# Performance work log

Hardware: AMD Instinct MI355X
Metric: run time of the kernel (lower is better)

Reference implementation:

```python
import jax, jax.numpy as jnp
import numpy as np
from functools import partial
from jax import lax

B, K, CLIP_DIM, SBERT_DIM, D_MODEL, R_RANK, ATTN_DIM, PMAX = 128, 1024, 768, 384, 256, 64, 256, 8
RHO = 0.35

def _normalize(x, axis=-1, eps=1e-12):
    return x / jnp.maximum(jnp.linalg.norm(x, axis=axis, keepdims=True), eps)

def _build_graph():
    rng = np.random.default_rng(0)
    pid = np.zeros((K, PMAX), np.int32)
    pm = np.zeros((K, PMAX), bool)
    for i in range(K - 1):  # node i's parents are in (i, K); root = K-1 has none
        n = int(rng.integers(1, PMAX + 1))
        n = min(n, K - 1 - i)
        cands = rng.choice(np.arange(i + 1, K), size=n, replace=False)
        pid[i, :n] = cands
        pm[i, :n] = True
    order = np.arange(K - 1, -1, -1, dtype=np.int32)  # parents before children
    return jnp.asarray(pid), jnp.asarray(pm), jnp.asarray(order)

def setup_inputs() -> dict:
    key = jax.random.key(0)
    ks = iter(jax.random.split(key, 32))
    r = lambda shape, s=0.02: jax.random.normal(next(ks), shape, jnp.float32) * s
    pid, pm, order = _build_graph()
    return {
        "t_clip": jax.random.normal(next(ks), (B, CLIP_DIM), jnp.float32),
        "v_clip": jax.random.normal(next(ks), (B, CLIP_DIM), jnp.float32),
        "concept_sbert": jax.random.normal(next(ks), (K, SBERT_DIM), jnp.float32),
        "Wt": r((CLIP_DIM, D_MODEL)), "bt": jnp.zeros((D_MODEL,)),
        "Wv": r((CLIP_DIM, D_MODEL)), "bv": jnp.zeros((D_MODEL,)),
        "Wc": r((SBERT_DIM, D_MODEL)), "bc": jnp.zeros((D_MODEL,)),
        "Wp1": r((3 * D_MODEL, 2 * D_MODEL)), "bp1": jnp.zeros((2 * D_MODEL,)),
        "Wp2": r((2 * D_MODEL, D_MODEL)), "bp2": jnp.zeros((D_MODEL,)),
        "Wm1": r((3 * D_MODEL, 2 * D_MODEL)), "bm1": jnp.zeros((2 * D_MODEL,)),
        "Wm2": r((2 * D_MODEL, D_MODEL)), "bm2": jnp.zeros((D_MODEL,)),
        "tau_logits": jnp.zeros((K,)),
        "U": r((D_MODEL, R_RANK)), "V": r((D_MODEL, R_RANK)),
        "Wg1": r((SBERT_DIM, R_RANK)), "bg1": jnp.zeros((R_RANK,)),
        "Wg2": r((R_RANK, R_RANK)), "bg2": jnp.zeros((R_RANK,)),
        "w_out": r((K, R_RANK)), "b_out": jnp.zeros((K,)),
        "concept_q": r((K, ATTN_DIM)),
        "parents_idx": pid, "parents_mask": pm, "order": order,
    }

def _forward(t_clip, v_clip, concept_sbert, Wt, bt, Wv, bv, Wc, bc,
             Wp1, bp1, Wp2, bp2, Wm1, bm1, Wm2, bm2, tau_logits,
             U, V, Wg1, bg1, Wg2, bg2, w_out, b_out, concept_q,
             parents_idx, parents_mask, order):
    gelu = partial(jax.nn.gelu, approximate=False)  # torch nn.GELU default = exact erf
    t = _normalize(t_clip) @ Wt + bt                 # [B, D]
    v = _normalize(v_clip) @ Wv + bv                 # [B, D]
    d = concept_sbert @ Wc + bc                      # [K, D]
    # x = [v, t, d] broadcast to [B, K, 3D]
    x = jnp.concatenate([
        jnp.broadcast_to(v[:, None, :], (t.shape[0], K, D_MODEL)),
        jnp.broadcast_to(t[:, None, :], (t.shape[0], K, D_MODEL)),
        jnp.broadcast_to(d[None, :, :], (t.shape[0], K, D_MODEL)),
    ], axis=-1)
    h_plus = gelu(x @ Wp1 + bp1) @ Wp2 + bp2
    h_minus = gelu(x @ Wm1 + bm1) @ Wm2 + bm2
    tau = jax.nn.sigmoid(tau_logits)[None, :, None]
    h = tau * h_plus + (1.0 - tau) * h_minus         # [B, K, D]
    u = jnp.einsum('bkd,dr->bkr', h, U)
    vv = jnp.einsum('bkd,dr->bkr', h, V)
    g = gelu(concept_sbert @ Wg1 + bg1) @ Wg2 + bg2  # [K, R]
    inter = u * vv * g[None, :, :]
    logits = jnp.einsum('bkr,kr->bk', inter, w_out) + b_out[None, :]
    p = jax.nn.sigmoid(logits)                        # [B, K]
    # --- top-down hierarchical attention + multiplicative aggregation ---
    q = _normalize(concept_q)                         # [K, A]
    def step(p_hat, node):
        par = parents_idx[node]                       # [P] int
        m = parents_mask[node]                        # [P] bool
        scores = jnp.where(m, q[par] @ q[node], -1e9)
        alpha = jax.nn.softmax(scores)                # [P]
        vals = p_hat[:, par]                          # [B, P] gather of parent probs
        prod = jnp.prod(jnp.where(m[None, :], alpha[None, :] * vals, 1.0), axis=-1)
        new = jnp.where(m.any(), RHO * p[:, node] + (1.0 - RHO) * prod, p_hat[:, node])
        return p_hat.at[:, node].set(new), None       # scatter write
    p_hat, _ = lax.scan(step, p, order)
    return p_hat

def reference(t_clip, v_clip, concept_sbert, Wt, bt, Wv, bv, Wc, bc,
              Wp1, bp1, Wp2, bp2, Wm1, bm1, Wm2, bm2, tau_logits,
              U, V, Wg1, bg1, Wg2, bg2, w_out, b_out, concept_q,
              parents_idx, parents_mask, order):
    return _forward(t_clip, v_clip, concept_sbert, Wt, bt, Wv, bv, Wc, bc,
                    Wp1, bp1, Wp2, bp2, Wm1, bm1, Wm2, bm2, tau_logits,
                    U, V, Wg1, bg1, Wg2, bg2, w_out, b_out, concept_q,
                    parents_idx, parents_mask, order)
```

## Files before the change

### kernel.cpp

```cpp
#include <hip/hip_runtime.h>
#include <math.h>

typedef __attribute__((ext_vector_type(8))) short short8;
typedef __attribute__((ext_vector_type(4))) float float4v;
typedef __attribute__((ext_vector_type(2))) float float2v;

struct P {
  const float *t_clip, *v_clip, *sbert;
  const float *Wt, *bt, *Wv, *bv, *Wc, *bc;
  const float *Wp1, *bp1, *Wp2, *bp2, *Wm1, *bm1, *Wm2, *bm2;
  const float *tau_logits, *U, *V, *Wg1, *bg1, *Wg2, *bg2, *w_out, *b_out, *concept_q;
  const int *pid;
  float *vt32;
  unsigned short *vtbf;
  unsigned short *dbf;
  unsigned short *w1upP, *w1upM;
  unsigned short *w1lowP, *w1lowM;
  unsigned short *Ctp, *Ctm;
  unsigned short *Wpk, *Wmk;
  float *Ap, *Am;
  float *biasPM, *tau, *gw, *aprod;
  unsigned short *parS;
  int *sorted, *lvlStart, *nlev;
  float *pOut;
};

__device__ __forceinline__ unsigned short bf16ru(float f) {
    unsigned u = __float_as_uint(f);
    u += 0x7fffu + ((u >> 16) & 1u);
    return (unsigned short)(u >> 16);
}

__device__ __forceinline__ unsigned packpair(float2v a, unsigned c) {
    float2v cb;
    cb.x = __uint_as_float(c << 16);
    cb.y = __uint_as_float(c & 0xffff0000u);
    float2v x = a + cb;
    float2v t = x * x;
    float2v i = t * (-0.06649038f) + 0.39894228f;
    float2v p = x * i + 0.5f;
    float2v g = x * p;
    union { float2v f; unsigned u[2]; } gu; gu.f = g;
    return __builtin_amdgcn_perm(gu.u[1], gu.u[0], 0x07060302u);
}


__device__ void tv_f(const P& a, int rel, float* sm) {
    int sel = rel & 1, ct = (rel >> 1) & 1, bt8 = rel >> 2;
    float* xrow = sm;
    float* scale = sm + 6144;
    int tid = threadIdx.x;
    const float* X = sel ? a.t_clip : a.v_clip;
    int b0 = bt8 * 8;
    for (int r = 0; r < 8; ++r)
        for (int i = tid; i < 768; i += 256)
            xrow[r * 768 + i] = X[(size_t)(b0 + r) * 768 + i];
    __syncthreads();
    {
        int r = tid >> 5, l = tid & 31;
        float ss = 0.f;
        for (int i = l; i < 768; i += 32) { float v = xrow[r * 768 + i]; ss = fmaf(v, v, ss); }
        for (int mk = 16; mk; mk >>= 1) ss += __shfl_xor(ss, mk);
        if (l == 0) scale[r] = 1.0f / fmaxf(sqrtf(ss), 1e-12f);
    }
    __syncthreads();
    int col = ct * 128 + (tid & 127);
    int rg = tid >> 7;
    const float* W = sel ? a.Wt : a.Wv;
    const float* bias = sel ? a.bt : a.bv;
    float acc[4] = {};
    for (int d = 0; d < 768; ++d) {
        float w = W[(size_t)d * 256 + col];
        const float* xr = xrow + (rg * 4) * 768 + d;
        acc[0] = fmaf(xr[0],    w, acc[0]);
        acc[1] = fmaf(xr[768],  w, acc[1]);
        acc[2] = fmaf(xr[1536], w, acc[2]);
        acc[3] = fmaf(xr[2304], w, acc[3]);
    }
    int vtcol = sel * 256 + col;
    float bb = bias[col];
#pragma unroll
    for (int r = 0; r < 4; ++r) {
        int b = b0 + rg * 4 + r;
        float y = acc[r] * scale[rg * 4 + r] + bb;
        a.vt32[(size_t)b * 512 + vtcol] = y;
        a.vtbf[(size_t)(b >> 4) * 8192 + (vtcol >> 5) * 512 + ((vtcol >> 3) & 3) * 128
               + (b & 15) * 8 + (vtcol & 7)] = bf16ru(y);
    }
}

__device__ void d_f(const P& a, int rel, float* sm) {
    int r0 = rel * 8;
    int tid = threadIdx.x;
    for (int i = tid; i < 3072; i += 256) sm[i] = a.sbert[(size_t)r0 * 384 + i];
    __syncthreads();
    float acc[8] = {};
    int col = tid;
    for (int d = 0; d < 384; ++d) {
        float w = a.Wc[(size_t)d * 256 + col];
#pragma unroll
        for (int r = 0; r < 8; ++r) acc[r] = fmaf(sm[r * 384 + d], w, acc[r]);
    }
    float bb = a.bc[col];
#pragma unroll
    for (int r = 0; r < 8; ++r) {
        int row = r0 + r;
        a.dbf[(size_t)(row >> 4) * 4096 + (col >> 5) * 512 + ((col >> 3) & 3) * 128
              + (row & 15) * 8 + (col & 7)] = bf16ru(acc[r] + bb);
    }
}

__device__ void wcv_f(const P& a, int rel, float* smf) {
    unsigned short* wl = (unsigned short*)smf;
    int mat = rel & 1, rb = rel >> 1;
    int r0 = rb * 16;
    const float* W1 = mat ? a.Wm1 : a.Wp1;
    int tid = threadIdx.x;
    for (int i = tid; i < 8192; i += 256)
        wl[i] = bf16ru(W1[(size_t)r0 * 512 + i]);
    __syncthreads();
    unsigned short* dst; int K16, kbase;
    if (r0 < 512) { dst = mat ? a.w1upM : a.w1upP;  K16 = 8192; kbase = r0; }
    else          { dst = mat ? a.w1lowM : a.w1lowP; K16 = 4096; kbase = r0 - 512; }
    for (int i = tid; i < 1024; i += 256) {
        int kg = i >> 9, n = i & 511;
        int k0 = kbase + kg * 8;
        ushort4 o0, o1;
        o0.x = wl[(kg * 8 + 0) * 512 + n]; o0.y = wl[(kg * 8 + 1) * 512 + n];
        o0.z = wl[(kg * 8 + 2) * 512 + n]; o0.w = wl[(kg * 8 + 3) * 512 + n];
        o1.x = wl[(kg * 8 + 4) * 512 + n]; o1.y = wl[(kg * 8 + 5) * 512 + n];
        o1.z = wl[(kg * 8 + 6) * 512 + n]; o1.w = wl[(kg * 8 + 7) * 512 + n];
        size_t off = (size_t)(n >> 4) * K16 + (k0 >> 5) * 512 + ((k0 >> 3) & 3) * 128 + (n & 15) * 8;
        *(ushort4*)&dst[off]     = o0;
        *(ushort4*)&dst[off + 4] = o1;
    }
}

__device__ void packW_f(const P& a, int rel, float* smf) {
    float* w2l = smf;
    int mat = rel >> 6, jb = rel & 63;
    int j0 = jb * 8;
    const float* W2 = mat ? a.Wm2 : a.Wp2;
    unsigned short* outP = mat ? a.Wmk : a.Wpk;
    int tid = threadIdx.x;
    for (int i = tid; i < 2048; i += 256) w2l[i] = W2[(size_t)j0 * 256 + i];
    __syncthreads();
    int c = tid & 127, jg = tid >> 7;
    float acc[4] = {};
    const float* uv = (c < 64) ? (a.U + c) : (a.V + (c - 64));
    for (int d = 0; d < 256; ++d) {
        float u = uv[(size_t)d * 64];
        const float* wr = w2l + (jg * 4) * 256 + d;
        acc[0] = fmaf(wr[0],   u, acc[0]);
        acc[1] = fmaf(wr[256], u, acc[1]);
        acc[2] = fmaf(wr[512], u, acc[2]);
        acc[3] = fmaf(wr[768], u, acc[3]);
    }
#pragma unroll
    for (int r = 0; r < 4; ++r) {
        int j = j0 + jg * 4 + r;
        size_t o = (size_t)(j >> 5) * 4096 + (c >> 4) * 512 + ((j >> 3) & 3) * 128 + (c & 15) * 8 + (j & 7);
        outP[o] = bf16ru(acc[r]);
    }
}

__device__ void gw_f(const P& a, int rel, float* sm) {
    float* sb = sm;
    float* hid = sm + 6144;
    int k0 = rel * 16;
    int tid = threadIdx.x;
    for (int i = tid; i < 6144; i += 256) sb[i] = a.sbert[(size_t)k0 * 384 + i];
    __syncthreads();
    int col = tid & 63, rg = tid >> 6;
    float bg = a.bg1[col];
    float acc[4] = {bg, bg, bg, bg};
    for (int d = 0; d < 384; ++d) {
        float w = a.Wg1[(size_t)d * 64 + col];
        const float* xr = sb + (rg * 4) * 384 + d;
        acc[0] = fmaf(xr[0],    w, acc[0]);
        acc[1] = fmaf(xr[384],  w, acc[1]);
        acc[2] = fmaf(xr[768],  w, acc[2]);
        acc[3] = fmaf(xr[1152], w, acc[3]);
    }
#pragma unroll
    for (int r = 0; r < 4; ++r)
        hid[(rg * 4 + r) * 64 + col] = 0.5f * acc[r] * (1.0f + erff(acc[r] * 0.7071067811865475f));
    __syncthreads();
    float bg2v = a.bg2[col];
    float a2[4] = {bg2v, bg2v, bg2v, bg2v};
    for (int d = 0; d < 64; ++d) {
        float w = a.Wg2[(size_t)d * 64 + col];
        const float* hr = hid + (rg * 4) * 64 + d;
        a2[0] = fmaf(hr[0],   w, a2[0]);
        a2[1] = fmaf(hr[64],  w, a2[1]);
        a2[2] = fmaf(hr[128], w, a2[2]);
        a2[3] = fmaf(hr[192], w, a2[3]);
    }
#pragma unroll
    for (int r = 0; r < 4; ++r) {
        int k = k0 + rg * 4 + r;
        a.gw[(size_t)k * 64 + col] = a2[r] * a.w_out[(size_t)k * 64 + col];
    }
}

__device__ void alpha_f(const P& a, int blk) {
    int t = threadIdx.x, wv = t >> 6, lane = t & 63;
    int node = blk * 4 + wv;
    int slot = lane >> 3, e = lane & 7;
    int par = a.pid[node * 8 + slot];
    const float4* qk = (const float4*)(a.concept_q + (size_t)node * 256);
    const float4* qp = (const float4*)(a.concept_q + (size_t)par * 256);
    float dq = 0, np = 0, ns = 0;
#pragma unroll
    for (int i = 0; i < 8; ++i) {
        float4 x = qp[e * 8 + i], y = qk[e * 8 + i];
        dq += x.x * y.x + x.y * y.y + x.z * y.z + x.w * y.w;
        np += x.x * x.x + x.y * x.y + x.z * x.z + x.w * x.w;
        ns += y.x * y.x + y.y * y.y + y.z * y.z + y.w * y.w;
    }
#pragma unroll
    for (int mk = 1; mk <= 4; mk <<= 1) {
        dq += __shfl_xor(dq, mk); np += __shfl_xor(np, mk); ns += __shfl_xor(ns, mk);
    }
    float score = dq / fmaxf(sqrtf(np) * sqrtf(ns), 1e-24f);
    float sc[8]; int pv[8];
#pragma unroll
    for (int s = 0; s < 8; ++s) { sc[s] = __shfl(score, s * 8); pv[s] = __shfl(par, s * 8); }
    float mx = -1e30f;
#pragma unroll
    for (int s = 0; s < 8; ++s) if (pv[s] != 0) mx = fmaxf(mx, sc[s]);
    float sum = 0.f;
#pragma unroll
    for (int s = 0; s < 8; ++s) sum += (pv[s] != 0) ? expf(sc[s] - mx) : 0.0f;
    float ap = 1.0f;
#pragma unroll
    for (int s = 0; s < 8; ++s) if (pv[s] != 0) ap *= expf(sc[s] - mx) / sum;
    if (lane == 0) a.aprod[node] = ap;
    if (e == 0) a.parS[node * 8 + slot] = (par != 0) ? (unsigned short)par : (unsigned short)1024;
}

__device__ void misc_f(const P& a, int g) {
    int t = threadIdx.x;
    if (g == 0) {
        int c = t & 127;
        const float* bb = (t < 128) ? a.bp2 : a.bm2;
        const float* uv = (c < 64) ? (a.U + c) : (a.V + (c - 64));
        float acc = 0.f;
        for (int d = 0; d < 256; ++d) acc = fmaf(bb[d], uv[(size_t)d * 64], acc);
        a.biasPM[t] = acc;
    } else {
        int k = (g - 1) * 256 + t;
        a.tau[k] = 1.0f / (1.0f + expf(-a.tau_logits[k]));
    }
}

__device__ void levels_f(const P& a, int* smemI) {
    volatile int* lvl = smemI;
    int* cnt  = smemI + 1024;
    int* ofs  = smemI + 2048;
    int* ping = smemI + 3072;
    int* pong = smemI + 3328;
    int* mflag = smemI + 3584;
    int t = threadIdx.x;
    int par[4][8]; int hasm[4];
#pragma unroll
    for (int r = 0; r < 4; ++r) {
        int n = t * 4 + r, h = 0;
#pragma unroll
        for (int s = 0; s < 8; ++s) { int p = a.pid[n * 8 + s]; par[r][s] = p; h |= (p != 0); }
        hasm[r] = h; lvl[n] = 0;
    }
    if (t == 0) mflag[1] = 0;
    __syncthreads();
    for (int round = 0; round < 200; ++round) {
        if (t == 0) mflag[0] = 0;
        __syncthreads();
        int ch = 0;
        for (int sub = 0; sub < 8; ++sub) {
#pragma unroll
            for (int r = 0; r < 4; ++r) {
                if (!hasm[r]) continue;
                int mx = 0;
#pragma unroll
                for (int s = 0; s < 8; ++s) { int p = par[r][s]; if (p) mx = max(mx, lvl[p]); }
                int nl = mx + 1;
                if (nl > lvl[t * 4 + r]) { lvl[t * 4 + r] = nl; ch = 1; }
            }
        }
        if (ch) mflag[0] = 1;
        __syncthreads();
        if (mflag[0] == 0) break;
    }
    int lm = 0;
    for (int r = 0; r < 4; ++r) lm = max(lm, lvl[t * 4 + r]);
    atomicMax(&mflag[1], lm);
    for (int r = 0; r < 4; ++r) cnt[t * 4 + r] = 0;
    __syncthreads();
    for (int r = 0; r < 4; ++r) atomicAdd(&cnt[lvl[t * 4 + r]], 1);
    __syncthreads();
    int c0 = cnt[t * 4], c1 = cnt[t * 4 + 1], c2 = cnt[t * 4 + 2], c3 = cnt[t * 4 + 3];
    ping[t] = c0 + c1 + c2 + c3;
    __syncthreads();
    int* src = ping; int* dst = pong;
    for (int off = 1; off < 256; off <<= 1) {
        int v = src[t];
        if (t >= off) v += src[t - off];
        dst[t] = v;
        __syncthreads();
        int* tmp = src; src = dst; dst = tmp;
    }
    int excl = (t == 0) ? 0 : src[t - 1];
    ofs[t * 4] = excl; ofs[t * 4 + 1] = excl + c0;
    ofs[t * 4 + 2] = excl + c0 + c1; ofs[t * 4 + 3] = excl + c0 + c1 + c2;
#pragma unroll
    for (int r = 0; r < 4; ++r) a.lvlStart[t * 4 + r] = ofs[t * 4 + r];
    if (t == 0) { a.lvlStart[1024] = 1024; a.nlev[0] = mflag[1] + 1; }
    __syncthreads();
    for (int r = 0; r < 4; ++r) {
        int n = t * 4 + r;
        int pos = atomicAdd(&ofs[lvl[n]], 1);
        a.sorted[pos] = n;
    }
}

__global__ void __launch_bounds__(256) prep1_kernel(P a) {
    __shared__ float smem[7200];
    int bid = blockIdx.x;
    if (bid == 0) { levels_f(a, (int*)smem); return; }
    bid -= 1;
    if (bid < 64) { tv_f(a, bid, smem); return; }
    bid -= 64;
    if (bid < 128) { d_f(a, bid, smem); return; }
    bid -= 128;
    if (bid < 96) { wcv_f(a, bid, smem); return; }
    bid -= 96;
    if (bid < 128) { packW_f(a, bid, smem); return; }
    bid -= 128;
    if (bid < 64) { gw_f(a, bid, smem); return; }
    bid -= 64;
    if (bid < 256) { alpha_f(a, bid); return; }
    bid -= 256;
    misc_f(a, bid);
}

__global__ void __launch_bounds__(256) prep2_kernel(P a) {
    int bid = blockIdx.x;
    int tid = threadIdx.x;
    int wv = tid >> 6, lane = tid & 63;
    int m = lane & 15, quad = lane >> 4;
    if (bid < 128) {
        int mat = bid & 1, mt = (bid >> 1) & 15, ntile = bid >> 5;
        const unsigned short* A = a.dbf + (size_t)(mt * 4 + wv) * 4096 + quad * 128 + m * 8;
        const unsigned short* B = (mat ? a.w1lowM : a.w1lowP) + (size_t)quad * 128 + m * 8;
        unsigned short* Ct = mat ? a.Ctm : a.Ctp;
        float4v acc[8];
#pragma unroll
        for (int i = 0; i < 8; ++i) acc[i] = (float4v)0.0f;
        for (int s = 0; s < 8; ++s) {
            short8 af = *(const short8*)(A + s * 512);
#pragma unroll
            for (int nt = 0; nt < 8; ++nt) {
                short8 bf = *(const short8*)(B + (size_t)(ntile * 8 + nt) * 4096 + s * 512);
                acc[nt] = __builtin_amdgcn_mfma_f32_16x16x32_bf16(af, bf, acc[nt], 0, 0, 0);
            }
        }
        int rowg = mt * 4 + wv;
        int rl = quad * 4;
#pragma unroll
        for (int nt = 0; nt < 8; ++nt) {
            int j = ntile * 128 + nt * 16 + m;
            size_t base = (size_t)rowg * 8192 + (j >> 5) * 512 + ((j >> 3) & 3) * 128 + (j & 7);
#pragma unroll
            for (int rr = 0; rr < 4; ++rr)
                Ct[base + (rl + rr) * 8] = bf16ru(acc[nt][rr]);
        }
    } else {
        int rel = bid - 128;
        int mat = rel & 1, mt = (rel >> 1) & 1, ntile = rel >> 2;
        const unsigned short* A = a.vtbf + (size_t)(mt * 4 + wv) * 8192 + quad * 128 + m * 8;
        const unsigned short* B = (mat ? a.w1upM : a.w1upP) + (size_t)quad * 128 + m * 8;
        const float* bias = mat ? a.bm1 : a.bp1;
        float* out = mat ? a.Am : a.Ap;
        float4v acc[8];
#pragma unroll
        for (int i = 0; i < 8; ++i) acc[i] = (float4v)0.0f;
        for (int s = 0; s < 16; ++s) {
            short8 af = *(const short8*)(A + s * 512);
#pragma unroll
            for (int nt = 0; nt < 8; ++nt) {
                short8 bf = *(const short8*)(B + (size_t)(ntile * 8 + nt) * 8192 + s * 512);
                acc[nt] = __builtin_amdgcn_mfma_f32_16x16x32_bf16(af, bf, acc[nt], 0, 0, 0);
            }
        }
        int b0r = mt * 64 + wv * 16 + quad * 4;
#pragma unroll
        for (int nt = 0; nt < 8; ++nt) {
            int j = ntile * 128 + nt * 16 + m;
            float bb = bias[j];
#pragma unroll
            for (int rr = 0; rr < 4; ++rr)
                out[(size_t)(b0r + rr) * 512 + j] = acc[nt][rr] + bb;
        }
    }
}

__global__ void __launch_bounds__(512, 2) main_kernel(P a) {
    __shared__ float apL[4096];
    __shared__ float xbuf[4 * 4 * 64 * 8];
    int tid = threadIdx.x;
    int wv2 = tid >> 6, lane = tid & 63;
    int mat = wv2 >> 2, sub = wv2 & 3;
    int m = lane & 15, quad = lane >> 4;
    int b0 = (blockIdx.x >> 4) * 4;
    int k0 = (blockIdx.x & 15) << 6;

    for (int i = tid; i < 1024; i += 512) {
        int arr = i >> 7, off = i & 127;
        const float* src = ((arr >> 2) ? a.Am : a.Ap) + (size_t)(b0 + (arr & 3)) * 512;
        ((float4*)apL)[i] = ((const float4*)src)[off];
    }
    __syncthreads();

    const unsigned short* W  = mat ? a.Wmk : a.Wpk;
    const unsigned short* Ct = mat ? a.Ctm : a.Ctp;
    const float* aL = apL + mat * 2048;
    int kt = (k0 >> 4) + sub;
    const char* ctB = (const char*)Ct + (size_t)kt * 16384 + quad * 256 + m * 16;
    const char* wB  = (const char*)W + quad * 256 + m * 16;

    float4v acc[4][8];
#pragma unroll
    for (int b = 0; b < 4; ++b)
#pragma unroll
        for (int i = 0; i < 8; ++i) acc[b][i] = (float4v)0.0f;

    uint4 crN = *(const uint4*)(ctB);
    for (int n = 0; n < 16; ++n) {
        uint4 cr = crN;
        if (n < 15) crN = *(const uint4*)(ctB + (n + 1) * 1024);
        union { uint4 u; short8 s; } fa[4];
        const float* aj = aL + n * 32 + quad * 8;
#pragma unroll
        for (int b = 0; b < 4; ++b) {
            float4v x0 = *(const float4v*)(aj + b * 512);
            float4v x1 = *(const float4v*)(aj + b * 512 + 4);
            float2v v;
            v.x = x0[0]; v.y = x0[1]; fa[b].u.x = packpair(v, cr.x);
            v.x = x0[2]; v.y = x0[3]; fa[b].u.y = packpair(v, cr.y);
            v.x = x1[0]; v.y = x1[1]; fa[b].u.z = packpair(v, cr.z);
            v.x = x1[2]; v.y = x1[3]; fa[b].u.w = packpair(v, cr.w);
        }
        const char* wn = wB + n * 8192;
#pragma unroll
        for (int nt = 0; nt < 8; ++nt) {
            short8 wf = *(const short8*)(wn + nt * 1024);
            acc[0][nt] = __builtin_amdgcn_mfma_f32_16x16x32_bf16(fa[0].s, wf, acc[0][nt], 0, 0, 0);
            acc[1][nt] = __builtin_amdgcn_mfma_f32_16x16x32_bf16(fa[1].s, wf, acc[1][nt], 0, 0, 0);
            acc[2][nt] = __builtin_amdgcn_mfma_f32_16x16x32_bf16(fa[2].s, wf, acc[2][nt], 0, 0, 0);
            acc[3][nt] = __builtin_amdgcn_mfma_f32_16x16x32_bf16(fa[3].s, wf, acc[3][nt], 0, 0, 0);
        }
    }

    int kk[4]; float tv[4];
#pragma unroll
    for (int r = 0; r < 4; ++r) { kk[r] = k0 + sub * 16 + quad * 4 + r; tv[r] = a.tau[kk[r]]; }
    float lsum[4][4] = {};
    float* xb = xbuf + ((sub * 4) * 64 + lane) * 8;
#pragma unroll
    for (int t4 = 0; t4 < 4; ++t4) {
        __syncthreads();
        if (mat == 1) {
#pragma unroll
            for (int b = 0; b < 4; ++b) {
                float* d = xb + b * 512;
#pragma unroll
                for (int r = 0; r < 4; ++r) { d[r] = acc[b][t4][r]; d[4 + r] = acc[b][t4 + 4][r]; }
            }
        }
        __syncthreads();
        if (mat == 0) {
            int cU = t4 * 16 + m, cV = cU + 64;
            float bPu = a.biasPM[cU], bMu = a.biasPM[128 + cU];
            float bPv = a.biasPM[cV], bMv = a.biasPM[128 + cV];
#pragma unroll
            for (int b = 0; b < 4; ++b) {
                const float* d = xb + b * 512;
#pragma unroll
                for (int r = 0; r < 4; ++r) {
                    float g = a.gw[(size_t)kk[r] * 64 + cU];
                    float u  = tv[r] * (acc[b][t4][r] + bPu)     + (1.0f - tv[r]) * (d[r] + bMu);
                    float vx = tv[r] * (acc[b][t4 + 4][r] + bPv) + (1.0f - tv[r]) * (d[4 + r] + bMv);
                    lsum[b][r] = fmaf(u * vx, g, lsum[b][r]);
                }
            }
        }
    }
    if (mat == 0) {
#pragma unroll
        for (int r = 0; r < 4; ++r) {
            float bo = a.b_out[kk[r]];
#pragma unroll
            for (int b = 0; b < 4; ++b) {
                float s = lsum[b][r];
                s += __shfl_xor(s, 1); s += __shfl_xor(s, 2); s += __shfl_xor(s, 4); s += __shfl_xor(s, 8);
                if (m == 0)
                    a.pOut[(size_t)(b0 + b) * 1024 + kk[r]] = 1.0f / (1.0f + expf(-(s + bo)));
            }
        }
    }
}

#define PH_STRIDE 1056
__global__ void __launch_bounds__(256) scan_kernel(P a) {
    __shared__ float ph[4 * PH_STRIDE];
    __shared__ float aprodL[1024];
    __shared__ unsigned short parL[8192];
    __shared__ short sortedL[1024];
    __shared__ int lvlStartL[1025];
    int t = threadIdx.x;
    int b0 = blockIdx.x * 4;
    for (int i = t; i < 1024; i += 256) ((uint4*)parL)[i] = ((const uint4*)a.parS)[i];
    for (int i = t; i < 1024; i += 256) {
        aprodL[i] = a.aprod[i];
        sortedL[i] = (short)a.sorted[i];
        lvlStartL[i] = a.lvlStart[i];
    }
    if (t == 0) lvlStartL[1024] = 1024;
    for (int i = t; i < 4096; i += 256) {
        int bb = i >> 10, k = i & 1023;
        ph[bb * PH_STRIDE + k] = a.pOut[(size_t)(b0 + bb) * 1024 + k];
    }
    if (t < 4) ph[t * PH_STRIDE + 1024] = 1.0f;
    __syncthreads();
    int nlev = a.nlev[0];
    int w = t >> 6, lane = t & 63;
    float* myph = ph + w * PH_STRIDE;
    for (int L = 1; L < nlev; ++L) {
        int s0 = lvlStartL[L], s1 = lvlStartL[L + 1];
        for (int i = s0 + lane; i < s1; i += 64) {
            int node = sortedL[i];
            ushort4 pA = *(const ushort4*)&parL[node * 8];
            ushort4 pB = *(const ushort4*)&parL[node * 8 + 4];
            float prod = aprodL[node];
            prod *= myph[pA.x] * myph[pA.y];
            prod *= myph[pA.z] * myph[pA.w];
            prod *= myph[pB.x] * myph[pB.y];
            prod *= myph[pB.z] * myph[pB.w];
            myph[node] = fmaf(0.35f, myph[node], 0.65f * prod);
        }
    }
    __syncthreads();
    for (int i = t; i < 4096; i += 256) {
        int bb = i >> 10, k = i & 1023;
        a.pOut[(size_t)(b0 + bb) * 1024 + k] = ph[bb * PH_STRIDE + k];
    }
}

extern "C" void kernel_launch(void* const* d_in, const int* in_sizes, int n_in,
                              void* d_out, int out_size, void* d_ws, size_t ws_size,
                              hipStream_t stream) {
    P a;
    a.t_clip = (const float*)d_in[0];
    a.v_clip = (const float*)d_in[1];
    a.sbert  = (const float*)d_in[2];
    a.Wt  = (const float*)d_in[3];  a.bt  = (const float*)d_in[4];
    a.Wv  = (const float*)d_in[5];  a.bv  = (const float*)d_in[6];
    a.Wc  = (const float*)d_in[7];  a.bc  = (const float*)d_in[8];
    a.Wp1 = (const float*)d_in[9];  a.bp1 = (const float*)d_in[10];
    a.Wp2 = (const float*)d_in[11]; a.bp2 = (const float*)d_in[12];
    a.Wm1 = (const float*)d_in[13]; a.bm1 = (const float*)d_in[14];
    a.Wm2 = (const float*)d_in[15]; a.bm2 = (const float*)d_in[16];
    a.tau_logits = (const float*)d_in[17];
    a.U   = (const float*)d_in[18]; a.V   = (const float*)d_in[19];
    a.Wg1 = (const float*)d_in[20]; a.bg1 = (const float*)d_in[21];
    a.Wg2 = (const float*)d_in[22]; a.bg2 = (const float*)d_in[23];
    a.w_out = (const float*)d_in[24]; a.b_out = (const float*)d_in[25];
    a.concept_q = (const float*)d_in[26];
    a.pid = (const int*)d_in[27];

    char* w = (char*)d_ws;
    a.vt32   = (float*)(w + 0);
    a.vtbf   = (unsigned short*)(w + 262144);
    a.dbf    = (unsigned short*)(w + 393216);
    a.w1upP  = (unsigned short*)(w + 917504);
    a.w1upM  = (unsigned short*)(w + 1441792);
    a.w1lowP = (unsigned short*)(w + 1966080);
    a.w1lowM = (unsigned short*)(w + 2228224);
    a.Ctp    = (unsigned short*)(w + 2490368);
    a.Ctm    = (unsigned short*)(w + 3538944);
    a.Wpk    = (unsigned short*)(w + 4587520);
    a.Wmk    = (unsigned short*)(w + 4718592);
    a.Ap     = (float*)(w + 4849664);
    a.Am     = (float*)(w + 5111808);
    a.biasPM = (float*)(w + 5373952);
    a.tau    = (float*)(w + 5374976);
    a.gw     = (float*)(w + 5379072);
    a.parS   = (unsigned short*)(w + 5641216);
    a.aprod  = (float*)(w + 5657600);
    a.sorted = (int*)(w + 5661696);
    a.lvlStart = (int*)(w + 5665792);
    a.nlev     = (int*)(w + 5670144);
    a.pOut = (float*)d_out;

    prep1_kernel<<<742, 256, 0, stream>>>(a);
    prep2_kernel<<<144, 256, 0, stream>>>(a);
    main_kernel<<<512, 512, 0, stream>>>(a);
    scan_kernel<<<32, 256, 0, stream>>>(a);
}
```

Measured before the change: 286.9 us.

## Vectorize prep GEMVs, split prep2 tiles, stage main weights via LDS double buffer

```diff
diff --git a/kernel.cpp b/kernel.cpp
--- a/kernel.cpp
+++ b/kernel.cpp
@@ -31,6 +31,11 @@
     return (unsigned short)(u >> 16);
 }
 
+__device__ __forceinline__ void glds16(const void* g, void* l) {
+    __builtin_amdgcn_global_load_lds((const __attribute__((address_space(1))) unsigned int*)g,
+                                     (__attribute__((address_space(3))) unsigned int*)l, 16, 0, 0);
+}
+
 __device__ __forceinline__ unsigned packpair(float2v a, unsigned c) {
     float2v cb;
     cb.x = __uint_as_float(c << 16);
@@ -46,7 +51,7 @@
 
 
 __device__ void tv_f(const P& a, int rel, float* sm) {
-    int sel = rel & 1, ct = (rel >> 1) & 1, bt8 = rel >> 2;
+    int sel = rel & 1, bt8 = rel >> 1;
     float* xrow = sm;
     float* scale = sm + 6144;
     int tid = threadIdx.x;
@@ -64,28 +69,35 @@
         if (l == 0) scale[r] = 1.0f / fmaxf(sqrtf(ss), 1e-12f);
     }
     __syncthreads();
-    int col = ct * 128 + (tid & 127);
-    int rg = tid >> 7;
+    int col4 = (tid & 63) * 4, rg = tid >> 6;
     const float* W = sel ? a.Wt : a.Wv;
     const float* bias = sel ? a.bt : a.bv;
-    float acc[4] = {};
+    float acc[2][4] = {};
+    const float* xr0 = xrow + (rg * 2) * 768;
+    const float* xr1 = xr0 + 768;
     for (int d = 0; d < 768; ++d) {
-        float w = W[(size_t)d * 256 + col];
-        const float* xr = xrow + (rg * 4) * 768 + d;
-        acc[0] = fmaf(xr[0],    w, acc[0]);
-        acc[1] = fmaf(xr[768],  w, acc[1]);
-        acc[2] = fmaf(xr[1536], w, acc[2]);
-        acc[3] = fmaf(xr[2304], w, acc[3]);
-    }
-    int vtcol = sel * 256 + col;
-    float bb = bias[col];
-#pragma unroll
-    for (int r = 0; r < 4; ++r) {
-        int b = b0 + rg * 4 + r;
-        float y = acc[r] * scale[rg * 4 + r] + bb;
-        a.vt32[(size_t)b * 512 + vtcol] = y;
-        a.vtbf[(size_t)(b >> 4) * 8192 + (vtcol >> 5) * 512 + ((vtcol >> 3) & 3) * 128
-               + (b & 15) * 8 + (vtcol & 7)] = bf16ru(y);
+        float4 w = *(const float4*)&W[(size_t)d * 256 + col4];
+        float x0 = xr0[d], x1 = xr1[d];
+        acc[0][0] = fmaf(x0, w.x, acc[0][0]); acc[0][1] = fmaf(x0, w.y, acc[0][1]);
+        acc[0][2] = fmaf(x0, w.z, acc[0][2]); acc[0][3] = fmaf(x0, w.w, acc[0][3]);
+        acc[1][0] = fmaf(x1, w.x, acc[1][0]); acc[1][1] = fmaf(x1, w.y, acc[1][1]);
+        acc[1][2] = fmaf(x1, w.z, acc[1][2]); acc[1][3] = fmaf(x1, w.w, acc[1][3]);
+    }
+    float4 bb = *(const float4*)&bias[col4];
+    int vtcol = sel * 256 + col4;
+#pragma unroll
+    for (int rr = 0; rr < 2; ++rr) {
+        int b = b0 + rg * 2 + rr;
+        float sc = scale[rg * 2 + rr];
+        float4 o;
+        o.x = acc[rr][0] * sc + bb.x; o.y = acc[rr][1] * sc + bb.y;
+        o.z = acc[rr][2] * sc + bb.z; o.w = acc[rr][3] * sc + bb.w;
+        *(float4*)&a.vt32[(size_t)b * 512 + vtcol] = o;
+        ushort4 ob;
+        ob.x = bf16ru(o.x); ob.y = bf16ru(o.y); ob.z = bf16ru(o.z); ob.w = bf16ru(o.w);
+        size_t idx = (size_t)(b >> 4) * 8192 + (vtcol >> 5) * 512 + ((vtcol >> 3) & 3) * 128
+                   + (b & 15) * 8 + (vtcol & 7);
+        *(ushort4*)&a.vtbf[idx] = ob;
     }
 }
 
@@ -94,19 +106,28 @@
     int tid = threadIdx.x;
     for (int i = tid; i < 3072; i += 256) sm[i] = a.sbert[(size_t)r0 * 384 + i];
     __syncthreads();
-    float acc[8] = {};
-    int col = tid;
+    int col4 = (tid & 63) * 4, rg = tid >> 6;
+    float acc[2][4] = {};
+    const float* x0p = sm + (rg * 2) * 384;
+    const float* x1p = x0p + 384;
     for (int d = 0; d < 384; ++d) {
-        float w = a.Wc[(size_t)d * 256 + col];
-#pragma unroll
-        for (int r = 0; r < 8; ++r) acc[r] = fmaf(sm[r * 384 + d], w, acc[r]);
-    }
-    float bb = a.bc[col];
-#pragma unroll
-    for (int r = 0; r < 8; ++r) {
-        int row = r0 + r;
-        a.dbf[(size_t)(row >> 4) * 4096 + (col >> 5) * 512 + ((col >> 3) & 3) * 128
-              + (row & 15) * 8 + (col & 7)] = bf16ru(acc[r] + bb);
+        float4 w = *(const float4*)&a.Wc[(size_t)d * 256 + col4];
+        float x0 = x0p[d], x1 = x1p[d];
+        acc[0][0] = fmaf(x0, w.x, acc[0][0]); acc[0][1] = fmaf(x0, w.y, acc[0][1]);
+        acc[0][2] = fmaf(x0, w.z, acc[0][2]); acc[0][3] = fmaf(x0, w.w, acc[0][3]);
+        acc[1][0] = fmaf(x1, w.x, acc[1][0]); acc[1][1] = fmaf(x1, w.y, acc[1][1]);
+        acc[1][2] = fmaf(x1, w.z, acc[1][2]); acc[1][3] = fmaf(x1, w.w, acc[1][3]);
+    }
+    float4 bb = *(const float4*)&a.bc[col4];
+#pragma unroll
+    for (int rr = 0; rr < 2; ++rr) {
+        int row = r0 + rg * 2 + rr;
+        ushort4 ob;
+        ob.x = bf16ru(acc[rr][0] + bb.x); ob.y = bf16ru(acc[rr][1] + bb.y);
+        ob.z = bf16ru(acc[rr][2] + bb.z); ob.w = bf16ru(acc[rr][3] + bb.w);
+        size_t idx = (size_t)(row >> 4) * 4096 + (col4 >> 5) * 512 + ((col4 >> 3) & 3) * 128
+                   + (row & 15) * 8 + (col4 & 7);
+        *(ushort4*)&a.dbf[idx] = ob;
     }
 }
 
@@ -116,8 +137,13 @@
     int r0 = rb * 16;
     const float* W1 = mat ? a.Wm1 : a.Wp1;
     int tid = threadIdx.x;
-    for (int i = tid; i < 8192; i += 256)
-        wl[i] = bf16ru(W1[(size_t)r0 * 512 + i]);
+    for (int it = 0; it < 8; ++it) {
+        int i4 = (it * 256 + tid) * 4;
+        float4 w = *(const float4*)&W1[(size_t)r0 * 512 + i4];
+        ushort4 o;
+        o.x = bf16ru(w.x); o.y = bf16ru(w.y); o.z = bf16ru(w.z); o.w = bf16ru(w.w);
+        *(ushort4*)&wl[i4] = o;
+    }
     __syncthreads();
     unsigned short* dst; int K16, kbase;
     if (r0 < 512) { dst = mat ? a.w1upM : a.w1upP;  K16 = 8192; kbase = r0; }
@@ -328,8 +354,8 @@
     int bid = blockIdx.x;
     if (bid == 0) { levels_f(a, (int*)smem); return; }
     bid -= 1;
-    if (bid < 64) { tv_f(a, bid, smem); return; }
-    bid -= 64;
+    if (bid < 32) { tv_f(a, bid, smem); return; }
+    bid -= 32;
     if (bid < 128) { d_f(a, bid, smem); return; }
     bid -= 128;
     if (bid < 96) { wcv_f(a, bid, smem); return; }
@@ -348,54 +374,54 @@
     int tid = threadIdx.x;
     int wv = tid >> 6, lane = tid & 63;
     int m = lane & 15, quad = lane >> 4;
-    if (bid < 128) {
+    if (bid < 256) {
         int mat = bid & 1, mt = (bid >> 1) & 15, ntile = bid >> 5;
         const unsigned short* A = a.dbf + (size_t)(mt * 4 + wv) * 4096 + quad * 128 + m * 8;
         const unsigned short* B = (mat ? a.w1lowM : a.w1lowP) + (size_t)quad * 128 + m * 8;
         unsigned short* Ct = mat ? a.Ctm : a.Ctp;
-        float4v acc[8];
-#pragma unroll
-        for (int i = 0; i < 8; ++i) acc[i] = (float4v)0.0f;
+        float4v acc[4];
+#pragma unroll
+        for (int i = 0; i < 4; ++i) acc[i] = (float4v)0.0f;
         for (int s = 0; s < 8; ++s) {
             short8 af = *(const short8*)(A + s * 512);
 #pragma unroll
-            for (int nt = 0; nt < 8; ++nt) {
-                short8 bf = *(const short8*)(B + (size_t)(ntile * 8 + nt) * 4096 + s * 512);
+            for (int nt = 0; nt < 4; ++nt) {
+                short8 bf = *(const short8*)(B + (size_t)(ntile * 4 + nt) * 4096 + s * 512);
                 acc[nt] = __builtin_amdgcn_mfma_f32_16x16x32_bf16(af, bf, acc[nt], 0, 0, 0);
             }
         }
         int rowg = mt * 4 + wv;
         int rl = quad * 4;
 #pragma unroll
-        for (int nt = 0; nt < 8; ++nt) {
-            int j = ntile * 128 + nt * 16 + m;
+        for (int nt = 0; nt < 4; ++nt) {
+            int j = ntile * 64 + nt * 16 + m;
             size_t base = (size_t)rowg * 8192 + (j >> 5) * 512 + ((j >> 3) & 3) * 128 + (j & 7);
 #pragma unroll
             for (int rr = 0; rr < 4; ++rr)
                 Ct[base + (rl + rr) * 8] = bf16ru(acc[nt][rr]);
         }
     } else {
-        int rel = bid - 128;
+        int rel = bid - 256;
         int mat = rel & 1, mt = (rel >> 1) & 1, ntile = rel >> 2;
         const unsigned short* A = a.vtbf + (size_t)(mt * 4 + wv) * 8192 + quad * 128 + m * 8;
         const unsigned short* B = (mat ? a.w1upM : a.w1upP) + (size_t)quad * 128 + m * 8;
         const float* bias = mat ? a.bm1 : a.bp1;
         float* out = mat ? a.Am : a.Ap;
-        float4v acc[8];
-#pragma unroll
-        for (int i = 0; i < 8; ++i) acc[i] = (float4v)0.0f;
+        float4v acc[4];
+#pragma unroll
+        for (int i = 0; i < 4; ++i) acc[i] = (float4v)0.0f;
         for (int s = 0; s < 16; ++s) {
             short8 af = *(const short8*)(A + s * 512);
 #pragma unroll
-            for (int nt = 0; nt < 8; ++nt) {
-                short8 bf = *(const short8*)(B + (size_t)(ntile * 8 + nt) * 8192 + s * 512);
+            for (int nt = 0; nt < 4; ++nt) {
+                short8 bf = *(const short8*)(B + (size_t)(ntile * 4 + nt) * 8192 + s * 512);
                 acc[nt] = __builtin_amdgcn_mfma_f32_16x16x32_bf16(af, bf, acc[nt], 0, 0, 0);
             }
         }
         int b0r = mt * 64 + wv * 16 + quad * 4;
 #pragma unroll
-        for (int nt = 0; nt < 8; ++nt) {
-            int j = ntile * 128 + nt * 16 + m;
+        for (int nt = 0; nt < 4; ++nt) {
+            int j = ntile * 64 + nt * 16 + m;
             float bb = bias[j];
 #pragma unroll
             for (int rr = 0; rr < 4; ++rr)
@@ -406,7 +432,7 @@
 
 __global__ void __launch_bounds__(512, 2) main_kernel(P a) {
     __shared__ float apL[4096];
-    __shared__ float xbuf[4 * 4 * 64 * 8];
+    __shared__ char wbuf[2][16384];
     int tid = threadIdx.x;
     int wv2 = tid >> 6, lane = tid & 63;
     int mat = wv2 >> 2, sub = wv2 & 3;
@@ -419,14 +445,16 @@
         const float* src = ((arr >> 2) ? a.Am : a.Ap) + (size_t)(b0 + (arr & 3)) * 512;
         ((float4*)apL)[i] = ((const float4*)src)[off];
     }
-    __syncthreads();
-
-    const unsigned short* W  = mat ? a.Wmk : a.Wpk;
+
+    const char* wg = ((wv2 < 4) ? (const char*)a.Wpk : (const char*)a.Wmk)
+                   + (wv2 & 3) * 2048 + lane * 16;
+    char* wl0 = &wbuf[0][wv2 * 2048];
+    char* wl1 = &wbuf[1][wv2 * 2048];
+
     const unsigned short* Ct = mat ? a.Ctm : a.Ctp;
     const float* aL = apL + mat * 2048;
     int kt = (k0 >> 4) + sub;
     const char* ctB = (const char*)Ct + (size_t)kt * 16384 + quad * 256 + m * 16;
-    const char* wB  = (const char*)W + quad * 256 + m * 16;
 
     float4v acc[4][8];
 #pragma unroll
@@ -434,8 +462,17 @@
 #pragma unroll
         for (int i = 0; i < 8; ++i) acc[b][i] = (float4v)0.0f;
 
+    glds16(wg, wl0);
+    glds16(wg + 1024, wl0 + 1024);
     uint4 crN = *(const uint4*)(ctB);
+    __syncthreads();
+
     for (int n = 0; n < 16; ++n) {
+        if (n < 15) {
+            char* dst = ((n + 1) & 1) ? wl1 : wl0;
+            glds16(wg + (n + 1) * 8192, dst);
+            glds16(wg + (n + 1) * 8192 + 1024, dst + 1024);
+        }
         uint4 cr = crN;
         if (n < 15) crN = *(const uint4*)(ctB + (n + 1) * 1024);
         union { uint4 u; short8 s; } fa[4];
@@ -450,31 +487,35 @@
             v.x = x1[0]; v.y = x1[1]; fa[b].u.z = packpair(v, cr.z);
             v.x = x1[2]; v.y = x1[3]; fa[b].u.w = packpair(v, cr.w);
         }
-        const char* wn = wB + n * 8192;
+        const char* wB = &wbuf[n & 1][0] + mat * 8192 + quad * 256 + m * 16;
 #pragma unroll
         for (int nt = 0; nt < 8; ++nt) {
-            short8 wf = *(const short8*)(wn + nt * 1024);
+            short8 wf = *(const short8*)(wB + nt * 1024);
             acc[0][nt] = __builtin_amdgcn_mfma_f32_16x16x32_bf16(fa[0].s, wf, acc[0][nt], 0, 0, 0);
             acc[1][nt] = __builtin_amdgcn_mfma_f32_16x16x32_bf16(fa[1].s, wf, acc[1][nt], 0, 0, 0);
             acc[2][nt] = __builtin_amdgcn_mfma_f32_16x16x32_bf16(fa[2].s, wf, acc[2][nt], 0, 0, 0);
             acc[3][nt] = __builtin_amdgcn_mfma_f32_16x16x32_bf16(fa[3].s, wf, acc[3][nt], 0, 0, 0);
         }
-    }
-
+        __syncthreads();
+    }
+
+    float* xbuf = (float*)wbuf;
     int kk[4]; float tv[4];
 #pragma unroll
     for (int r = 0; r < 4; ++r) { kk[r] = k0 + sub * 16 + quad * 4 + r; tv[r] = a.tau[kk[r]]; }
     float lsum[4][4] = {};
-    float* xb = xbuf + ((sub * 4) * 64 + lane) * 8;
 #pragma unroll
     for (int t4 = 0; t4 < 4; ++t4) {
         __syncthreads();
         if (mat == 1) {
 #pragma unroll
             for (int b = 0; b < 4; ++b) {
-                float* d = xb + b * 512;
-#pragma unroll
-                for (int r = 0; r < 4; ++r) { d[r] = acc[b][t4][r]; d[4 + r] = acc[b][t4 + 4][r]; }
+                int slot = (sub * 4 + b) * 64 + lane;
+#pragma unroll
+                for (int r = 0; r < 4; ++r) {
+                    xbuf[r * 1024 + slot]       = acc[b][t4][r];
+                    xbuf[(r + 4) * 1024 + slot] = acc[b][t4 + 4][r];
+                }
             }
         }
         __syncthreads();
@@ -484,12 +525,14 @@
             float bPv = a.biasPM[cV], bMv = a.biasPM[128 + cV];
 #pragma unroll
             for (int b = 0; b < 4; ++b) {
-                const float* d = xb + b * 512;
+                int slot = (sub * 4 + b) * 64 + lane;
 #pragma unroll
                 for (int r = 0; r < 4; ++r) {
                     float g = a.gw[(size_t)kk[r] * 64 + cU];
-                    float u  = tv[r] * (acc[b][t4][r] + bPu)     + (1.0f - tv[r]) * (d[r] + bMu);
-                    float vx = tv[r] * (acc[b][t4 + 4][r] + bPv) + (1.0f - tv[r]) * (d[4 + r] + bMv);
+                    float u  = tv[r] * (acc[b][t4][r] + bPu)
+                             + (1.0f - tv[r]) * (xbuf[r * 1024 + slot] + bMu);
+                    float vx = tv[r] * (acc[b][t4 + 4][r] + bPv)
+                             + (1.0f - tv[r]) * (xbuf[(r + 4) * 1024 + slot] + bMv);
                     lsum[b][r] = fmaf(u * vx, g, lsum[b][r]);
                 }
             }
@@ -602,8 +645,8 @@
     a.nlev     = (int*)(w + 5670144);
     a.pOut = (float*)d_out;
 
-    prep1_kernel<<<742, 256, 0, stream>>>(a);
-    prep2_kernel<<<144, 256, 0, stream>>>(a);
+    prep1_kernel<<<710, 256, 0, stream>>>(a);
+    prep2_kernel<<<288, 256, 0, stream>>>(a);
     main_kernel<<<512, 512, 0, stream>>>(a);
     scan_kernel<<<32, 256, 0, stream>>>(a);
 }
```

Measured after the change: 261.8 us. 8.8% less time.
